# Kernel tuning notes

Measured on AMD Instinct MI355X. Metric: run time of the kernel, lower is better.

## Reference

```python
import jax, jax.numpy as jnp
import numpy as np

DIM = 1024
HEADS = 16
D_HEAD = 64
INNER = HEADS * D_HEAD  # 1024
FF_INNER = 4 * DIM      # 4096


def setup_inputs() -> dict:
    key = jax.random.key(0)
    ks = jax.random.split(key, 12)
    s = lambda fan_in: 1.0 / np.sqrt(fan_in)
    x = jax.random.normal(ks[0], (4, 1024, DIM), dtype=jnp.float32)
    context = jax.random.normal(ks[1], (4, 2048, DIM), dtype=jnp.float32)
    Wq = jax.random.normal(ks[2], (DIM, INNER), dtype=jnp.float32) * s(DIM)
    Wk = jax.random.normal(ks[3], (DIM, INNER), dtype=jnp.float32) * s(DIM)
    Wv = jax.random.normal(ks[4], (DIM, INNER), dtype=jnp.float32) * s(DIM)
    Wo = jax.random.normal(ks[5], (INNER, DIM), dtype=jnp.float32) * s(INNER)
    bo = jax.random.normal(ks[6], (DIM,), dtype=jnp.float32) * 0.01
    W1 = jax.random.normal(ks[7], (DIM, FF_INNER), dtype=jnp.float32) * s(DIM)
    b1 = jax.random.normal(ks[8], (FF_INNER,), dtype=jnp.float32) * 0.01
    W2 = jax.random.normal(ks[9], (FF_INNER, DIM), dtype=jnp.float32) * s(FF_INNER)
    b2 = jax.random.normal(ks[10], (DIM,), dtype=jnp.float32) * 0.01
    return {"x": x, "context": context, "Wq": Wq, "Wk": Wk, "Wv": Wv,
            "Wo": Wo, "bo": bo, "W1": W1, "b1": b1, "W2": W2, "b2": b2}


def _block(x, context, Wq, Wk, Wv, Wo, bo, W1, b1, W2, b2):
    B, Lq, _ = x.shape
    scale = 1.0 / np.sqrt(D_HEAD).astype(np.float32)
    # cross attention
    q = (x @ Wq).reshape(B, Lq, HEADS, D_HEAD)          # [B,Lq,H,D]
    k = (context @ Wk).reshape(B, -1, HEADS, D_HEAD)    # [B,Lk,H,D]
    v = (context @ Wv).reshape(B, -1, HEADS, D_HEAD)
    sim = jnp.einsum('bqhd,bkhd->bhqk', q, k) * scale   # [B,H,Lq,Lk]
    attn = jax.nn.softmax(sim, axis=-1)
    out = jnp.einsum('bhqk,bkhd->bqhd', attn, v).reshape(B, Lq, INNER)
    x = out @ Wo + bo + x
    # feedforward (exact GELU as in torch F.gelu default)
    h = jax.nn.gelu(x @ W1 + b1, approximate=False)
    return h @ W2 + b2 + x


def reference(x, context, Wq, Wk, Wv, Wo, bo, W1, b1, W2, b2):
    return _block(x, context, Wq, Wk, Wv, Wo, bo, W1, b1, W2, b2)
```

## Files before the change

### kernel.cpp

```cpp
#include <hip/hip_runtime.h>
#include <hip/hip_bf16.h>
#include <cmath>
#include <cstdint>

typedef short s16x8 __attribute__((ext_vector_type(8)));
typedef unsigned short u16x8 __attribute__((ext_vector_type(8)));
typedef unsigned short u16x4 __attribute__((ext_vector_type(4)));
typedef float f32x4 __attribute__((ext_vector_type(4)));

__device__ __forceinline__ float bf2f(uint16_t u) {
  union { uint32_t i; float f; } c; c.i = ((uint32_t)u) << 16; return c.f;
}
__device__ __forceinline__ uint16_t f2bf(float f) {
  union { float f; uint32_t i; } c; c.f = f;
  return (uint16_t)((c.i + 0x7FFFu + ((c.i >> 16) & 1u)) >> 16);
}
__device__ __forceinline__ uint32_t pkbf(float a, float b) {
  union { __hip_bfloat162 h; uint32_t u; } c;
  c.h = __float22bfloat162_rn(float2{a, b});
  return c.u;
}

__device__ __forceinline__ float gelu_exactf(float v) {
  const float x = v * 0.70710678118654752f;
  const float ax = fabsf(x);
  const float t = 1.0f / (1.0f + 0.3275911f * ax);
  const float poly = ((((1.061405429f * t - 1.453152027f) * t + 1.421413741f) * t
                      - 0.284496736f) * t + 0.254829592f) * t;
  const float e = __expf(-x * x);
  float er = 1.0f - poly * e;
  er = copysignf(er, x);
  return 0.5f * v * (1.0f + er);
}

__device__ __forceinline__ void gload16(const void* g, void* l) {
  __builtin_amdgcn_global_load_lds(
      (const __attribute__((address_space(1))) void*)g,
      (__attribute__((address_space(3))) void*)l, 16, 0, 0);
}

__device__ __forceinline__ bool sniff_is_bf16(const uint16_t* u16, int64_t n,
                                              int tid, int* s_cnt) {
  int cnt = 0;
#pragma unroll
  for (int j = 0; j < 4; j++) {
    int64_t idx = (((int64_t)(tid * 4 + j)) * 2) % n;
    idx &= ~(int64_t)1;
    uint32_t e = (u16[idx] >> 7) & 0xFF;
    cnt += (e >= 96 && e <= 144) ? 1 : 0;
  }
  if (tid == 0) *s_cnt = 0;
  __syncthreads();
  atomicAdd(s_cnt, cnt);
  __syncthreads();
  return (*s_cnt) * 10 > 1024 * 6;
}

__global__ __launch_bounds__(256) void prep_all(
    float* dout,
    const void* xr, const void* cr, const void* bor, const void* b1r, const void* b2r,
    const void* Wq, const void* Wk, const void* Wv, const void* Wo,
    const void* W1, const void* W2,
    uint16_t* xo, uint16_t* co, uint16_t* boo, uint16_t* b1o, uint16_t* b2o,
    uint16_t* WqT, uint16_t* WkT, uint16_t* WvT, uint16_t* WoT,
    uint16_t* W1T, uint16_t* W2T) {
  __shared__ int s_cnt;
  __shared__ uint16_t tile[64][65];
  const int id = blockIdx.x;
  const int tid = threadIdx.x;

  if (id < 1024) {
    float* p = dout + ((int64_t)id * 256 + tid) * 4;
#pragma unroll
    for (int i = 0; i < 4; i++)
      *(f32x4*)(p + (int64_t)i * 262144) = (f32x4){0.f, 0.f, 0.f, 0.f};
    return;
  }
  if (id < 4099) {
    const void* src; uint16_t* dst; int64_t tot; int64_t base; int nv;
    if (id < 2048)      { src = xr; dst = xo; tot = 4194304; base = (int64_t)(id - 1024) * 4096; nv = 4; }
    else if (id < 4096) { src = cr; dst = co; tot = 8388608; base = (int64_t)(id - 2048) * 4096; nv = 4; }
    else if (id == 4096){ src = bor; dst = boo; tot = 1024; base = 0; nv = 1; }
    else if (id == 4097){ src = b1r; dst = b1o; tot = 4096; base = 0; nv = 4; }
    else                { src = b2r; dst = b2o; tot = 1024; base = 0; nv = 1; }
    const bool is16 = sniff_is_bf16((const uint16_t*)src, tot, tid, &s_cnt);
    if (is16) {
      const uint64_t* s = (const uint64_t*)((const uint16_t*)src + base);
      uint64_t* d = (uint64_t*)(dst + base);
      for (int i = 0; i < nv; i++) d[i * 256 + tid] = s[i * 256 + tid];
    } else {
      const f32x4* s = (const f32x4*)((const float*)src + base);
      uint2* d = (uint2*)(dst + base);
      for (int i = 0; i < nv; i++) {
        f32x4 v = s[i * 256 + tid];
        uint2 o; o.x = pkbf(v[0], v[1]); o.y = pkbf(v[2], v[3]);
        d[i * 256 + tid] = o;
      }
    }
    return;
  }
  const int t0 = id - 4099;
  const void* src; uint16_t* dst; int R, C, bx, by;
  if (t0 < 1024) {
    const int wsel = t0 >> 8, t = t0 & 255;
    const void* srcs[4] = {Wq, Wk, Wv, Wo};
    uint16_t* dsts[4] = {WqT, WkT, WvT, WoT};
    src = srcs[wsel]; dst = dsts[wsel]; R = 1024; C = 1024; bx = t & 15; by = t >> 4;
  } else if (t0 < 2048) { int t = t0 - 1024; src = W1; dst = W1T; R = 1024; C = 4096; bx = t & 63; by = t >> 6; }
  else                  { int t = t0 - 2048; src = W2; dst = W2T; R = 4096; C = 1024; bx = t & 15; by = t >> 4; }
  const uint16_t* u16 = (const uint16_t*)src;
  const float* f32 = (const float*)src;
  const bool is16 = sniff_is_bf16(u16, (int64_t)R * C, tid, &s_cnt);
  const int c0 = bx * 64, r0 = by * 64;
  if (is16) {
    const int c8 = (tid & 7) * 8, r = tid >> 3;
#pragma unroll
    for (int ri = 0; ri < 2; ri++) {
      const int row = r + ri * 32;
      u16x8 v = *(const u16x8*)(u16 + (int64_t)(r0 + row) * C + c0 + c8);
#pragma unroll
      for (int j = 0; j < 8; j++) tile[c8 + j][row] = v[j];
    }
  } else {
    const int c4 = (tid & 15) * 4, r = tid >> 4;
#pragma unroll
    for (int ri = 0; ri < 4; ri++) {
      const int row = r + ri * 16;
      f32x4 v = *(const f32x4*)(f32 + (int64_t)(r0 + row) * C + c0 + c4);
#pragma unroll
      for (int j = 0; j < 4; j++) tile[c4 + j][row] = f2bf(v[j]);
    }
  }
  __syncthreads();
  const int rr8 = (tid & 7) * 8, cc = tid >> 3;
#pragma unroll
  for (int ci = 0; ci < 2; ci++) {
    const int col = cc + ci * 32;
    *(u16x8*)(dst + (int64_t)(c0 + col) * R + r0 + rr8) = *(const u16x8*)&tile[col][rr8];
  }
}

__global__ __launch_bounds__(256) void vtrans(
    const uint16_t* __restrict__ KVb, uint16_t* __restrict__ Vt) {
  __shared__ uint16_t tile[64][65];
  const int z = blockIdx.z;
  const uint16_t* in = KVb + (int64_t)z * 2048 * 2048 + 1024;
  uint16_t* out = Vt + (int64_t)z * 1024 * 2048;
  const int tid = threadIdx.x;
  const int c0 = blockIdx.x * 64, k0 = blockIdx.y * 64;
  const int c8 = (tid & 7) * 8, r = tid >> 3;
#pragma unroll
  for (int ri = 0; ri < 2; ri++) {
    const int krow = r + ri * 32;
    u16x8 v = *(const u16x8*)(in + (int64_t)(k0 + krow) * 2048 + c0 + c8);
#pragma unroll
    for (int j = 0; j < 8; j++) tile[c8 + j][krow] = v[j];
  }
  __syncthreads();
  const int k8 = (tid & 7) * 8, cc = tid >> 3;
#pragma unroll
  for (int ci = 0; ci < 2; ci++) {
    const int col = cc + ci * 32;
    *(u16x8*)(out + (int64_t)(c0 + col) * 2048 + k0 + k8) = *(const u16x8*)&tile[col][k8];
  }
}

#define BM 128
#define BN 128
#define BK 64

enum { EPI_NONE = 0, EPI_BIAS_RES = 1, EPI_BIAS_GELU = 2 };

template <int EPI, int RESF32, int OUTF32, int SPLITK>
__device__ __forceinline__ void gemm_body(
    const uint16_t* __restrict__ A, const uint16_t* __restrict__ Bt,
    void* __restrict__ Cv, const uint16_t* __restrict__ bias,
    const void* __restrict__ resid, int M, int N, int K_total,
    int m0, int n0, int zslice, uint16_t* As, uint16_t* Bs) {
  const int tid = threadIdx.x;
  const int w = tid >> 6, l = tid & 63;
  const int wu = __builtin_amdgcn_readfirstlane(w);
  const int wm = (w >> 1) * 64, wn = (w & 1) * 64;
  const int ls = l & 15, lg = l >> 4;
  const int K = (SPLITK > 1) ? (K_total / SPLITK) : K_total;
  const int kof = (SPLITK > 1) ? zslice * K : 0;

  const int sr = 8 * w + (l >> 3);
  const int koff = (((l & 7) ^ ((l >> 3) & 7)) * 8);
  const uint16_t* Ag = A + (int64_t)(m0 + sr) * K_total + kof + koff;
  const uint16_t* Bg = Bt + (int64_t)(n0 + sr) * K_total + kof + koff;
  const int64_t rstep = (int64_t)32 * K_total;

  uint16_t* lA = As + wu * 512;
  uint16_t* lB = Bs + wu * 512;

  f32x4 acc[4][4] = {};

  for (int kb = 0; kb < K; kb += BK) {
    __syncthreads();
#pragma unroll
    for (int r = 0; r < 4; r++) {
      gload16(Ag + r * rstep + kb, lA + r * 2048);
      gload16(Bg + r * rstep + kb, lB + r * 2048);
    }
    __syncthreads();
#pragma unroll
    for (int kk = 0; kk < 2; kk++) {
      s16x8 af[4], bfr[4];
#pragma unroll
      for (int i = 0; i < 4; i++) {
        const int row = wm + i * 16 + ls;
        af[i] = *(const s16x8*)&As[row * 64 + (((kk * 4 + lg) ^ (ls & 7)) * 8)];
      }
#pragma unroll
      for (int j = 0; j < 4; j++) {
        const int row = wn + j * 16 + ls;
        bfr[j] = *(const s16x8*)&Bs[row * 64 + (((kk * 4 + lg) ^ (ls & 7)) * 8)];
      }
#pragma unroll
      for (int i = 0; i < 4; i++)
#pragma unroll
        for (int j = 0; j < 4; j++)
          acc[i][j] = __builtin_amdgcn_mfma_f32_16x16x32_bf16(af[i], bfr[j], acc[i][j], 0, 0, 0);
    }
  }

#pragma unroll
  for (int i = 0; i < 4; i++) {
#pragma unroll
    for (int rr = 0; rr < 4; rr++) {
      const int64_t row = m0 + wm + i * 16 + lg * 4 + rr;
#pragma unroll
      for (int j = 0; j < 4; j++) {
        const int col = n0 + wn + j * 16 + ls;
        float v = acc[i][j][rr];
        if (EPI == EPI_BIAS_RES) {
          if (SPLITK <= 1 || zslice == 0) {
            const float rv = RESF32 ? ((const float*)resid)[row * N + col]
                                    : bf2f(((const uint16_t*)resid)[row * N + col]);
            v += bf2f(bias[col]) + rv;
          }
        } else if (EPI == EPI_BIAS_GELU) {
          v += bf2f(bias[col]);
          v = gelu_exactf(v);
        }
        if (SPLITK > 1)
          atomicAdd((float*)Cv + row * N + col, v);
        else if (OUTF32)
          ((float*)Cv)[row * N + col] = v;
        else
          ((uint16_t*)Cv)[row * N + col] = f2bf(v);
      }
    }
  }
}

template <int EPI, int RESF32, int OUTF32, int SPLITK>
__global__ __launch_bounds__(256, 4) void gemm_single(
    const uint16_t* __restrict__ A, const uint16_t* __restrict__ Bt,
    void* __restrict__ Cv, const uint16_t* __restrict__ bias,
    const void* __restrict__ resid, int M, int N, int K_total) {
  __shared__ alignas(16) uint16_t As[BM * BK];
  __shared__ alignas(16) uint16_t Bs[BN * BK];
  gemm_body<EPI, RESF32, OUTF32, SPLITK>(A, Bt, Cv, bias, resid, M, N, K_total,
                                         blockIdx.x * BM, blockIdx.y * BN,
                                         (int)blockIdx.z, As, Bs);
}

__global__ __launch_bounds__(256, 4) void gemm_qkv(
    const uint16_t* __restrict__ xA, const uint16_t* __restrict__ WqT,
    uint16_t* __restrict__ Qb,
    const uint16_t* __restrict__ ctxA, const uint16_t* __restrict__ KVWt,
    uint16_t* __restrict__ KVb) {
  __shared__ alignas(16) uint16_t As[BM * BK];
  __shared__ alignas(16) uint16_t Bs[BN * BK];
  const int id = blockIdx.x;
  if (id < 256) {
    gemm_body<EPI_NONE, 0, 0, 0>(xA, WqT, Qb, nullptr, nullptr, 4096, 1024, 1024,
                                 (id & 31) * BM, (id >> 5) * BN, 0, As, Bs);
  } else {
    const int t = id - 256;
    gemm_body<EPI_NONE, 0, 0, 0>(ctxA, KVWt, KVb, nullptr, nullptr, 8192, 2048, 1024,
                                 (t & 63) * BM, (t >> 6) * BN, 0, As, Bs);
  }
}

#define KLD 72
#define PLD 72

__global__ __launch_bounds__(256, 2) void attn_kernel(
    const uint16_t* __restrict__ Q,
    const uint16_t* __restrict__ KV,
    const uint16_t* __restrict__ Vt,
    uint16_t* __restrict__ O) {
  __shared__ alignas(16) uint16_t Ks[2][64 * KLD];
  __shared__ alignas(16) uint16_t Vts[2][64 * KLD];
  __shared__ alignas(16) uint16_t Ps[8][16 * PLD];

  const int tid = threadIdx.x;
  const int w = tid >> 6, l = tid & 63;
  const int ls = l & 15, lg = l >> 4;

  const int blk = blockIdx.x;
  const int bh = blk & 63;
  const int qb = blk >> 6;
  const int h = bh & 15, b = bh >> 4;

  const int64_t qrow0 = (int64_t)b * 1024 + qb * 128;
  const int hoff = h * 64;
  const uint16_t* Vtb = Vt + (int64_t)b * 1024 * 2048;

  const float sc = 0.125f * 1.4426950408889634f;

  s16x8 qf[2][2];
#pragma unroll
  for (int qq = 0; qq < 2; qq++)
#pragma unroll
    for (int ks = 0; ks < 2; ks++) {
      s16x8 r = *(const s16x8*)(Q + (qrow0 + w * 32 + qq * 16 + ls) * 1024 + hoff + ks * 32 + lg * 8);
#pragma unroll
      for (int j = 0; j < 8; j++)
        qf[qq][ks][j] = (short)f2bf(bf2f((uint16_t)r[j]) * sc);
    }

  s16x8 onef;
#pragma unroll
  for (int j = 0; j < 8; j++) onef[j] = (short)0x3F80;

  f32x4 oacc[2][4] = {};
  f32x4 lsacc[2] = {};

  const int srow = tid >> 3;
  const int sc8 = (tid & 7) * 8;
  const uint16_t* Kg = KV + ((int64_t)b * 2048 + srow) * 2048 + hoff + sc8;
  const uint16_t* Vg = Vtb + (int64_t)(hoff + srow) * 2048 + sc8;

  s16x8 rk0 = *(const s16x8*)(Kg);
  s16x8 rk1 = *(const s16x8*)(Kg + (int64_t)32 * 2048);
  s16x8 rv0 = *(const s16x8*)(Vg);
  s16x8 rv1 = *(const s16x8*)(Vg + (int64_t)32 * 2048);

  for (int kt = 0; kt < 2048; kt += 64) {
    const int bi = (kt >> 6) & 1;
    *(s16x8*)&Ks[bi][srow * KLD + sc8] = rk0;
    *(s16x8*)&Ks[bi][(srow + 32) * KLD + sc8] = rk1;
    *(s16x8*)&Vts[bi][srow * KLD + sc8] = rv0;
    *(s16x8*)&Vts[bi][(srow + 32) * KLD + sc8] = rv1;
    const int ktn = kt + 64;
    if (ktn < 2048) {
      rk0 = *(const s16x8*)(Kg + (int64_t)ktn * 2048);
      rk1 = *(const s16x8*)(Kg + (int64_t)(ktn + 32) * 2048);
      rv0 = *(const s16x8*)(Vg + ktn);
      rv1 = *(const s16x8*)(Vg + ktn + (int64_t)32 * 2048);
    }
    __syncthreads();

    f32x4 st[2][4];
    __builtin_amdgcn_s_setprio(1);
#pragma unroll
    for (int jn = 0; jn < 4; jn++) {
      f32x4 z = {0.f, 0.f, 0.f, 0.f};
      st[0][jn] = z; st[1][jn] = z;
#pragma unroll
      for (int ks = 0; ks < 2; ks++) {
        s16x8 kf = *(const s16x8*)&Ks[bi][(jn * 16 + ls) * KLD + ks * 32 + lg * 8];
        st[0][jn] = __builtin_amdgcn_mfma_f32_16x16x32_bf16(kf, qf[0][ks], st[0][jn], 0, 0, 0);
        st[1][jn] = __builtin_amdgcn_mfma_f32_16x16x32_bf16(kf, qf[1][ks], st[1][jn], 0, 0, 0);
      }
    }
    __builtin_amdgcn_s_setprio(0);

#pragma unroll
    for (int qq = 0; qq < 2; qq++)
#pragma unroll
      for (int jn = 0; jn < 4; jn++) {
        const float p0 = exp2f(st[qq][jn][0]);
        const float p1 = exp2f(st[qq][jn][1]);
        const float p2 = exp2f(st[qq][jn][2]);
        const float p3 = exp2f(st[qq][jn][3]);
        uint2 pk; pk.x = pkbf(p0, p1); pk.y = pkbf(p2, p3);
        *(uint2*)&Ps[w * 2 + qq][ls * PLD + jn * 16 + lg * 4] = pk;
      }

    __builtin_amdgcn_s_setprio(1);
#pragma unroll
    for (int ks = 0; ks < 2; ks++) {
      s16x8 pf0 = *(const s16x8*)&Ps[w * 2 + 0][ls * PLD + ks * 32 + lg * 8];
      s16x8 pf1 = *(const s16x8*)&Ps[w * 2 + 1][ls * PLD + ks * 32 + lg * 8];
#pragma unroll
      for (int jn = 0; jn < 4; jn++) {
        s16x8 vf = *(const s16x8*)&Vts[bi][(jn * 16 + ls) * KLD + ks * 32 + lg * 8];
        oacc[0][jn] = __builtin_amdgcn_mfma_f32_16x16x32_bf16(pf0, vf, oacc[0][jn], 0, 0, 0);
        oacc[1][jn] = __builtin_amdgcn_mfma_f32_16x16x32_bf16(pf1, vf, oacc[1][jn], 0, 0, 0);
      }
      lsacc[0] = __builtin_amdgcn_mfma_f32_16x16x32_bf16(pf0, onef, lsacc[0], 0, 0, 0);
      lsacc[1] = __builtin_amdgcn_mfma_f32_16x16x32_bf16(pf1, onef, lsacc[1], 0, 0, 0);
    }
    __builtin_amdgcn_s_setprio(0);
  }

#pragma unroll
  for (int qq = 0; qq < 2; qq++) {
#pragma unroll
    for (int rr = 0; rr < 4; rr++) {
      const float inv = 1.0f / lsacc[qq][rr];
      const int64_t row = qrow0 + w * 32 + qq * 16 + lg * 4 + rr;
#pragma unroll
      for (int jn = 0; jn < 4; jn++)
        O[row * 1024 + hoff + jn * 16 + ls] = f2bf(oacc[qq][jn][rr] * inv);
    }
  }
}

extern "C" void kernel_launch(void* const* d_in, const int* in_sizes, int n_in,
                              void* d_out, int out_size, void* d_ws, size_t ws_size,
                              hipStream_t stream) {
  const void* x_raw   = d_in[0];
  const void* ctx_raw = d_in[1];
  const void* Wq_raw  = d_in[2];
  const void* Wk_raw  = d_in[3];
  const void* Wv_raw  = d_in[4];
  const void* Wo_raw  = d_in[5];
  const void* bo_raw  = d_in[6];
  const void* W1_raw  = d_in[7];
  const void* b1_raw  = d_in[8];
  const void* W2_raw  = d_in[9];
  const void* b2_raw  = d_in[10];

  const int64_t Mi = 1 << 20;
  uint16_t* ws   = (uint16_t*)d_ws;
  uint16_t* WqT  = ws;
  uint16_t* KVWt = ws + 1 * Mi;
  uint16_t* WoT  = ws + 3 * Mi;
  uint16_t* W1T  = ws + 4 * Mi;
  uint16_t* W2T  = ws + 8 * Mi;
  uint16_t* bob  = ws + 12 * Mi;
  uint16_t* b1b  = ws + 12 * Mi + 1024;
  uint16_t* b2b  = ws + 12 * Mi + 5120;
  uint16_t* xb   = ws + 13 * Mi;
  uint16_t* AO   = ws + 13 * Mi;
  uint16_t* ctxb = ws + 17 * Mi;
  uint16_t* Vt   = ws + 17 * Mi;
  uint16_t* X1   = ws + 17 * Mi;
  uint16_t* Qb   = ws + 25 * Mi;
  uint16_t* KVb  = ws + 29 * Mi;
  uint16_t* Hb   = ws + 29 * Mi;

  const dim3 tb(256);
  prep_all<<<dim3(7171), tb, 0, stream>>>(
      (float*)d_out,
      x_raw, ctx_raw, bo_raw, b1_raw, b2_raw,
      Wq_raw, Wk_raw, Wv_raw, Wo_raw, W1_raw, W2_raw,
      xb, ctxb, bob, b1b, b2b,
      WqT, KVWt, KVWt + Mi, WoT, W1T, W2T);

  gemm_qkv<<<dim3(1280), tb, 0, stream>>>(xb, WqT, Qb, ctxb, KVWt, KVb);

  vtrans<<<dim3(16, 32, 4), tb, 0, stream>>>(KVb, Vt);

  attn_kernel<<<dim3(512), tb, 0, stream>>>(Qb, KVb, Vt, AO);

  gemm_single<EPI_BIAS_RES, 1, 0, 0><<<dim3(32, 8), tb, 0, stream>>>(
      AO, WoT, X1, bob, x_raw, 4096, 1024, 1024);
  gemm_single<EPI_BIAS_GELU, 0, 0, 0><<<dim3(32, 32), tb, 0, stream>>>(
      X1, W1T, Hb, b1b, nullptr, 4096, 4096, 1024);
  gemm_single<EPI_BIAS_RES, 0, 1, 4><<<dim3(32, 8, 4), tb, 0, stream>>>(
      Hb, W2T, d_out, b2b, X1, 4096, 1024, 4096);
}
```

Baseline: 418.4 us.

## Fuse V transpose into KV GEMM epilogue and replace atomic split-K with reduce

The KV projection epilogue now writes the V half directly in transposed layout, so the separate vtrans kernel is gone. Vt is placed in the output buffer to save workspace. The FF2 GEMM drops from 4-way atomic split-K to 2-way split-K with plain stores into two fp32 buffers, followed by a small reduce kernel that adds the partials, bias and residual. The output zero-fill in prep is removed. This trades a kernel launch and atomic traffic for strided transposed stores and an extra elementwise pass; the split-K partial reuses the weight workspace region.

```diff
diff --git a/kernel.cpp b/kernel.cpp
--- a/kernel.cpp
+++ b/kernel.cpp
@@ -57,7 +57,6 @@
 }
 
 __global__ __launch_bounds__(256) void prep_all(
-    float* dout,
     const void* xr, const void* cr, const void* bor, const void* b1r, const void* b2r,
     const void* Wq, const void* Wk, const void* Wv, const void* Wo,
     const void* W1, const void* W2,
@@ -69,19 +68,12 @@
   const int id = blockIdx.x;
   const int tid = threadIdx.x;
 
-  if (id < 1024) {
-    float* p = dout + ((int64_t)id * 256 + tid) * 4;
-#pragma unroll
-    for (int i = 0; i < 4; i++)
-      *(f32x4*)(p + (int64_t)i * 262144) = (f32x4){0.f, 0.f, 0.f, 0.f};
-    return;
-  }
-  if (id < 4099) {
+  if (id < 3075) {
     const void* src; uint16_t* dst; int64_t tot; int64_t base; int nv;
-    if (id < 2048)      { src = xr; dst = xo; tot = 4194304; base = (int64_t)(id - 1024) * 4096; nv = 4; }
-    else if (id < 4096) { src = cr; dst = co; tot = 8388608; base = (int64_t)(id - 2048) * 4096; nv = 4; }
-    else if (id == 4096){ src = bor; dst = boo; tot = 1024; base = 0; nv = 1; }
-    else if (id == 4097){ src = b1r; dst = b1o; tot = 4096; base = 0; nv = 4; }
+    if (id < 1024)      { src = xr; dst = xo; tot = 4194304; base = (int64_t)id * 4096; nv = 4; }
+    else if (id < 3072) { src = cr; dst = co; tot = 8388608; base = (int64_t)(id - 1024) * 4096; nv = 4; }
+    else if (id == 3072){ src = bor; dst = boo; tot = 1024; base = 0; nv = 1; }
+    else if (id == 3073){ src = b1r; dst = b1o; tot = 4096; base = 0; nv = 4; }
     else                { src = b2r; dst = b2o; tot = 1024; base = 0; nv = 1; }
     const bool is16 = sniff_is_bf16((const uint16_t*)src, tot, tid, &s_cnt);
     if (is16) {
@@ -99,7 +91,7 @@
     }
     return;
   }
-  const int t0 = id - 4099;
+  const int t0 = id - 3075;
   const void* src; uint16_t* dst; int R, C, bx, by;
   if (t0 < 1024) {
     const int wsel = t0 >> 8, t = t0 & 255;
@@ -140,41 +132,17 @@
   }
 }
 
-__global__ __launch_bounds__(256) void vtrans(
-    const uint16_t* __restrict__ KVb, uint16_t* __restrict__ Vt) {
-  __shared__ uint16_t tile[64][65];
-  const int z = blockIdx.z;
-  const uint16_t* in = KVb + (int64_t)z * 2048 * 2048 + 1024;
-  uint16_t* out = Vt + (int64_t)z * 1024 * 2048;
-  const int tid = threadIdx.x;
-  const int c0 = blockIdx.x * 64, k0 = blockIdx.y * 64;
-  const int c8 = (tid & 7) * 8, r = tid >> 3;
-#pragma unroll
-  for (int ri = 0; ri < 2; ri++) {
-    const int krow = r + ri * 32;
-    u16x8 v = *(const u16x8*)(in + (int64_t)(k0 + krow) * 2048 + c0 + c8);
-#pragma unroll
-    for (int j = 0; j < 8; j++) tile[c8 + j][krow] = v[j];
-  }
-  __syncthreads();
-  const int k8 = (tid & 7) * 8, cc = tid >> 3;
-#pragma unroll
-  for (int ci = 0; ci < 2; ci++) {
-    const int col = cc + ci * 32;
-    *(u16x8*)(out + (int64_t)(c0 + col) * 2048 + k0 + k8) = *(const u16x8*)&tile[col][k8];
-  }
-}
-
 #define BM 128
 #define BN 128
 #define BK 64
 
-enum { EPI_NONE = 0, EPI_BIAS_RES = 1, EPI_BIAS_GELU = 2 };
+enum { EPI_NONE = 0, EPI_BIAS_RES = 1, EPI_BIAS_GELU = 2, EPI_KV = 3 };
 
 template <int EPI, int RESF32, int OUTF32, int SPLITK>
 __device__ __forceinline__ void gemm_body(
     const uint16_t* __restrict__ A, const uint16_t* __restrict__ Bt,
-    void* __restrict__ Cv, const uint16_t* __restrict__ bias,
+    void* __restrict__ Cv, void* __restrict__ Cv2,
+    const uint16_t* __restrict__ bias,
     const void* __restrict__ resid, int M, int N, int K_total,
     int m0, int n0, int zslice, uint16_t* As, uint16_t* Bs) {
   const int tid = threadIdx.x;
@@ -225,6 +193,37 @@
     }
   }
 
+  if constexpr (EPI == EPI_KV) {
+    if (n0 >= 1024) {
+      uint16_t* VtB = (uint16_t*)Cv2 + (int64_t)(m0 >> 11) * 2097152;
+#pragma unroll
+      for (int i = 0; i < 4; i++) {
+        const int k0 = (m0 & 2047) + wm + i * 16 + lg * 4;
+#pragma unroll
+        for (int j = 0; j < 4; j++) {
+          const int c = n0 - 1024 + wn + j * 16 + ls;
+          uint2 pk;
+          pk.x = pkbf(acc[i][j][0], acc[i][j][1]);
+          pk.y = pkbf(acc[i][j][2], acc[i][j][3]);
+          *(uint2*)(VtB + (int64_t)c * 2048 + k0) = pk;
+        }
+      }
+    } else {
+#pragma unroll
+      for (int i = 0; i < 4; i++)
+#pragma unroll
+        for (int rr = 0; rr < 4; rr++) {
+          const int64_t row = m0 + wm + i * 16 + lg * 4 + rr;
+#pragma unroll
+          for (int j = 0; j < 4; j++) {
+            const int col = n0 + wn + j * 16 + ls;
+            ((uint16_t*)Cv)[row * N + col] = f2bf(acc[i][j][rr]);
+          }
+        }
+    }
+    return;
+  }
+
 #pragma unroll
   for (int i = 0; i < 4; i++) {
 #pragma unroll
@@ -235,18 +234,17 @@
         const int col = n0 + wn + j * 16 + ls;
         float v = acc[i][j][rr];
         if (EPI == EPI_BIAS_RES) {
-          if (SPLITK <= 1 || zslice == 0) {
-            const float rv = RESF32 ? ((const float*)resid)[row * N + col]
-                                    : bf2f(((const uint16_t*)resid)[row * N + col]);
-            v += bf2f(bias[col]) + rv;
-          }
+          const float rv = RESF32 ? ((const float*)resid)[row * N + col]
+                                  : bf2f(((const uint16_t*)resid)[row * N + col]);
+          v += bf2f(bias[col]) + rv;
         } else if (EPI == EPI_BIAS_GELU) {
           v += bf2f(bias[col]);
           v = gelu_exactf(v);
         }
-        if (SPLITK > 1)
-          atomicAdd((float*)Cv + row * N + col, v);
-        else if (OUTF32)
+        if (SPLITK > 1) {
+          float* Co = (float*)(zslice ? Cv2 : Cv);
+          Co[row * N + col] = v;
+        } else if (OUTF32)
           ((float*)Cv)[row * N + col] = v;
         else
           ((uint16_t*)Cv)[row * N + col] = f2bf(v);
@@ -258,11 +256,12 @@
 template <int EPI, int RESF32, int OUTF32, int SPLITK>
 __global__ __launch_bounds__(256, 4) void gemm_single(
     const uint16_t* __restrict__ A, const uint16_t* __restrict__ Bt,
-    void* __restrict__ Cv, const uint16_t* __restrict__ bias,
+    void* __restrict__ Cv, void* __restrict__ Cv2,
+    const uint16_t* __restrict__ bias,
     const void* __restrict__ resid, int M, int N, int K_total) {
   __shared__ alignas(16) uint16_t As[BM * BK];
   __shared__ alignas(16) uint16_t Bs[BN * BK];
-  gemm_body<EPI, RESF32, OUTF32, SPLITK>(A, Bt, Cv, bias, resid, M, N, K_total,
+  gemm_body<EPI, RESF32, OUTF32, SPLITK>(A, Bt, Cv, Cv2, bias, resid, M, N, K_total,
                                          blockIdx.x * BM, blockIdx.y * BN,
                                          (int)blockIdx.z, As, Bs);
 }
@@ -271,18 +270,36 @@
     const uint16_t* __restrict__ xA, const uint16_t* __restrict__ WqT,
     uint16_t* __restrict__ Qb,
     const uint16_t* __restrict__ ctxA, const uint16_t* __restrict__ KVWt,
-    uint16_t* __restrict__ KVb) {
+    uint16_t* __restrict__ KVb, uint16_t* __restrict__ Vt) {
   __shared__ alignas(16) uint16_t As[BM * BK];
   __shared__ alignas(16) uint16_t Bs[BN * BK];
   const int id = blockIdx.x;
   if (id < 256) {
-    gemm_body<EPI_NONE, 0, 0, 0>(xA, WqT, Qb, nullptr, nullptr, 4096, 1024, 1024,
+    gemm_body<EPI_NONE, 0, 0, 1>(xA, WqT, Qb, nullptr, nullptr, nullptr, 4096, 1024, 1024,
                                  (id & 31) * BM, (id >> 5) * BN, 0, As, Bs);
   } else {
     const int t = id - 256;
-    gemm_body<EPI_NONE, 0, 0, 0>(ctxA, KVWt, KVb, nullptr, nullptr, 8192, 2048, 1024,
-                                 (t & 63) * BM, (t >> 6) * BN, 0, As, Bs);
-  }
+    gemm_body<EPI_KV, 0, 0, 1>(ctxA, KVWt, KVb, Vt, nullptr, nullptr, 8192, 2048, 1024,
+                               (t & 63) * BM, (t >> 6) * BN, 0, As, Bs);
+  }
+}
+
+__global__ __launch_bounds__(256) void ff2_reduce(
+    float* __restrict__ dout, const float* __restrict__ p1,
+    const uint16_t* __restrict__ X1, const uint16_t* __restrict__ b2) {
+  const int64_t i0 = ((int64_t)blockIdx.x * 256 + threadIdx.x) * 8;
+  f32x4 d0 = *(const f32x4*)(dout + i0), d1 = *(const f32x4*)(dout + i0 + 4);
+  f32x4 q0 = *(const f32x4*)(p1 + i0),  q1 = *(const f32x4*)(p1 + i0 + 4);
+  u16x8 x = *(const u16x8*)(X1 + i0);
+  u16x8 bb = *(const u16x8*)(b2 + (i0 & 1023));
+  f32x4 r0, r1;
+#pragma unroll
+  for (int e = 0; e < 4; e++) {
+    r0[e] = d0[e] + q0[e] + bf2f(x[e]) + bf2f(bb[e]);
+    r1[e] = d1[e] + q1[e] + bf2f(x[e + 4]) + bf2f(bb[e + 4]);
+  }
+  *(f32x4*)(dout + i0) = r0;
+  *(f32x4*)(dout + i0 + 4) = r1;
 }
 
 #define KLD 72
@@ -433,6 +450,7 @@
   uint16_t* KVWt = ws + 1 * Mi;
   uint16_t* WoT  = ws + 3 * Mi;
   uint16_t* W1T  = ws + 4 * Mi;
+  float*    P1f  = (float*)ws;
   uint16_t* W2T  = ws + 8 * Mi;
   uint16_t* bob  = ws + 12 * Mi;
   uint16_t* b1b  = ws + 12 * Mi + 1024;
@@ -440,30 +458,28 @@
   uint16_t* xb   = ws + 13 * Mi;
   uint16_t* AO   = ws + 13 * Mi;
   uint16_t* ctxb = ws + 17 * Mi;
-  uint16_t* Vt   = ws + 17 * Mi;
   uint16_t* X1   = ws + 17 * Mi;
   uint16_t* Qb   = ws + 25 * Mi;
   uint16_t* KVb  = ws + 29 * Mi;
   uint16_t* Hb   = ws + 29 * Mi;
+  uint16_t* Vt   = (uint16_t*)d_out;
 
   const dim3 tb(256);
-  prep_all<<<dim3(7171), tb, 0, stream>>>(
-      (float*)d_out,
+  prep_all<<<dim3(6147), tb, 0, stream>>>(
       x_raw, ctx_raw, bo_raw, b1_raw, b2_raw,
       Wq_raw, Wk_raw, Wv_raw, Wo_raw, W1_raw, W2_raw,
       xb, ctxb, bob, b1b, b2b,
       WqT, KVWt, KVWt + Mi, WoT, W1T, W2T);
 
-  gemm_qkv<<<dim3(1280), tb, 0, stream>>>(xb, WqT, Qb, ctxb, KVWt, KVb);
-
-  vtrans<<<dim3(16, 32, 4), tb, 0, stream>>>(KVb, Vt);
+  gemm_qkv<<<dim3(1280), tb, 0, stream>>>(xb, WqT, Qb, ctxb, KVWt, KVb, Vt);
 
   attn_kernel<<<dim3(512), tb, 0, stream>>>(Qb, KVb, Vt, AO);
 
-  gemm_single<EPI_BIAS_RES, 1, 0, 0><<<dim3(32, 8), tb, 0, stream>>>(
-      AO, WoT, X1, bob, x_raw, 4096, 1024, 1024);
-  gemm_single<EPI_BIAS_GELU, 0, 0, 0><<<dim3(32, 32), tb, 0, stream>>>(
-      X1, W1T, Hb, b1b, nullptr, 4096, 4096, 1024);
-  gemm_single<EPI_BIAS_RES, 0, 1, 4><<<dim3(32, 8, 4), tb, 0, stream>>>(
-      Hb, W2T, d_out, b2b, X1, 4096, 1024, 4096);
-}
+  gemm_single<EPI_BIAS_RES, 1, 0, 1><<<dim3(32, 8), tb, 0, stream>>>(
+      AO, WoT, X1, nullptr, bob, x_raw, 4096, 1024, 1024);
+  gemm_single<EPI_BIAS_GELU, 0, 0, 1><<<dim3(32, 32), tb, 0, stream>>>(
+      X1, W1T, Hb, nullptr, b1b, nullptr, 4096, 4096, 1024);
+  gemm_single<EPI_NONE, 0, 1, 2><<<dim3(32, 8, 2), tb, 0, stream>>>(
+      Hb, W2T, d_out, P1f, nullptr, nullptr, 4096, 1024, 4096);
+  ff2_reduce<<<dim3(2048), tb, 0, stream>>>((float*)d_out, P1f, X1, b2b);
+}
```

Measured after the change: 376.9 us. 9.9% less time.
